# Performance work log

Measured on AMD Instinct MI355X. Metric: run time of the kernel, lower is better.

## Reference

```python
import jax, jax.numpy as jnp
import numpy as np

B, S, F = 128, 256, 40
H, D, NH, L, FF = 64, 128, 4, 2, 2048
REG, BIN, NW = 8, 1, 3
NEG = -1e9


def _ln(x, s, b, eps=1e-5):
    m = x.mean(-1, keepdims=True)
    v = ((x - m) ** 2).mean(-1, keepdims=True)
    return (x - m) / jnp.sqrt(v + eps) * s + b


def setup_inputs() -> dict:
    key = jax.random.key(0)
    ks = list(jax.random.split(key, 40))
    k = iter(ks)
    def rn(shape, s=0.05):
        return jax.random.normal(next(k), shape, jnp.float32) * s
    inp = {}
    inp['x'] = jax.random.normal(next(k), (B, S, F), jnp.float32)
    inp['mask'] = jnp.ones((B, S, F), jnp.float32)
    inp['delta'] = jax.random.uniform(next(k), (B, S, F), jnp.float32)
    # GRU params (torch layout: [3H, in], gates order r,z,n)
    inp['gru_w_ih'] = rn((3 * H, 3 * F))
    inp['gru_w_hh'] = rn((3 * H, H))
    inp['gru_b_ih'] = rn((3 * H,))
    inp['gru_b_hh'] = rn((3 * H,))
    inp['dm_w'] = rn((D, H)); inp['dm_b'] = rn((D,))
    # transformer layers stacked on leading dim L
    inp['in_proj_w'] = rn((L, 3 * D, D)); inp['in_proj_b'] = rn((L, 3 * D))
    inp['out_proj_w'] = rn((L, D, D)); inp['out_proj_b'] = rn((L, D))
    inp['lin1_w'] = rn((L, FF, D)); inp['lin1_b'] = rn((L, FF))
    inp['lin2_w'] = rn((L, D, FF)); inp['lin2_b'] = rn((L, D))
    inp['ln1_s'] = jnp.ones((L, D), jnp.float32); inp['ln1_b'] = jnp.zeros((L, D), jnp.float32)
    inp['ln2_s'] = jnp.ones((L, D), jnp.float32); inp['ln2_b'] = jnp.zeros((L, D), jnp.float32)
    inp['score_w'] = rn((1, D)); inp['score_b'] = rn((1,))
    inp['reg_w'] = rn((NW, REG, D)); inp['reg_b'] = rn((NW, REG))
    inp['bin_w'] = rn((NW, BIN, D)); inp['bin_b'] = rn((NW, BIN))
    inp['window_id'] = jax.random.randint(next(k), (B,), 0, NW, jnp.int32)
    return inp


def reference(x, mask, delta, gru_w_ih, gru_w_hh, gru_b_ih, gru_b_hh, dm_w, dm_b,
              in_proj_w, in_proj_b, out_proj_w, out_proj_b, lin1_w, lin1_b,
              lin2_w, lin2_b, ln1_s, ln1_b, ln2_s, ln2_b, score_w, score_b,
              reg_w, reg_b, bin_w, bin_b, window_id):
    inp = jnp.concatenate([x, mask, delta], -1)          # [B,S,3F]
    xw = inp @ gru_w_ih.T + gru_b_ih                      # [B,S,3H] precomputed input gates

    def step(h, xw_t):
        gh = h @ gru_w_hh.T + gru_b_hh
        xr, xz, xn = jnp.split(xw_t, 3, -1)
        hr, hz, hn = jnp.split(gh, 3, -1)
        r = jax.nn.sigmoid(xr + hr)
        zg = jax.nn.sigmoid(xz + hz)
        n = jnp.tanh(xn + r * hn)
        h_new = (1.0 - zg) * n + zg * h
        return h_new, h_new

    h0 = jnp.zeros((x.shape[0], H), x.dtype)
    _, hs = jax.lax.scan(step, h0, jnp.swapaxes(xw, 0, 1))  # [S,B,H]
    z = jnp.swapaxes(hs, 0, 1) @ dm_w.T + dm_b              # [B,S,D]

    time_mask = mask.sum(-1) > 0                            # [B,S] bool
    bias = jnp.where(time_mask[:, None, None, :], 0.0, NEG).astype(z.dtype)
    dh = D // NH
    scale = 1.0 / np.sqrt(dh)

    for l in range(L):  # post-LN torch TransformerEncoderLayer
        qkv = z @ in_proj_w[l].T + in_proj_b[l]
        q, k, v = jnp.split(qkv, 3, -1)
        q = q.reshape(B, S, NH, dh).transpose(0, 2, 1, 3)
        k = k.reshape(B, S, NH, dh).transpose(0, 2, 1, 3)
        v = v.reshape(B, S, NH, dh).transpose(0, 2, 1, 3)
        attn = jax.nn.softmax(jnp.einsum('bhqd,bhkd->bhqk', q, k) * scale + bias, -1)
        o = jnp.einsum('bhqk,bhkd->bhqd', attn, v).transpose(0, 2, 1, 3).reshape(B, S, D)
        z = _ln(z + (o @ out_proj_w[l].T + out_proj_b[l]), ln1_s[l], ln1_b[l])
        ff = jax.nn.relu(z @ lin1_w[l].T + lin1_b[l]) @ lin2_w[l].T + lin2_b[l]
        z = _ln(z + ff, ln2_s[l], ln2_b[l])

    scores = (z @ score_w.T + score_b)[..., 0]              # [B,S]
    scores = jnp.where(time_mask, scores, NEG)
    alpha = jax.nn.softmax(scores, 1)
    pooled = jnp.einsum('bsd,bs->bd', z, alpha)             # [B,D]

    # routed heads: gather 1-of-3 head weights per sample, batched matvec
    y_reg = jnp.einsum('bod,bd->bo', reg_w[window_id], pooled) + reg_b[window_id]
    y_bin = jnp.einsum('bod,bd->bo', bin_w[window_id], pooled) + bin_b[window_id]
    return (y_reg, y_bin)
```

## Files before the change

kernel.cpp:

```cpp
#include <hip/hip_runtime.h>

typedef __attribute__((ext_vector_type(8))) short short8;
typedef __attribute__((ext_vector_type(4))) float f32x4;
typedef unsigned short u16;

#define BB   128
#define SS   256
#define FIN  40
#define HH   64
#define DD   128
#define NHH  4
#define LL   2
#define NEGV (-1e9f)

__device__ __forceinline__ u16 f2b(float f) {
    unsigned u = __float_as_uint(f);
    return (u16)((u + 0x7FFFu + ((u >> 16) & 1u)) >> 16);
}
__device__ __forceinline__ float b2f(u16 u) {
    return __uint_as_float(((unsigned)u) << 16);
}

__global__ __launch_bounds__(256) void cvt_all_kernel(const float* __restrict__ dm_w,
                                                      const float* __restrict__ ip_w,
                                                      const float* __restrict__ op_w,
                                                      const float* __restrict__ l1_w,
                                                      const float* __restrict__ l2_w,
                                                      u16* __restrict__ o_dm, u16* __restrict__ o_ip,
                                                      u16* __restrict__ o_op, u16* __restrict__ o_l1,
                                                      u16* __restrict__ o_l2) {
    int blk = blockIdx.x;
    const float* s; u16* d; int off;
    if      (blk < 4)   { s = dm_w; d = o_dm; off = blk; }
    else if (blk < 52)  { s = ip_w; d = o_ip; off = blk - 4; }
    else if (blk < 68)  { s = op_w; d = o_op; off = blk - 52; }
    else if (blk < 324) { s = l1_w; d = o_l1; off = blk - 68; }
    else                { s = l2_w; d = o_l2; off = blk - 324; }
    int i = (off * 256 + threadIdx.x) * 8;
    float4 a = *(const float4*)&s[i];
    float4 b = *(const float4*)&s[i + 4];
    short8 o;
    o[0] = (short)f2b(a.x); o[1] = (short)f2b(a.y); o[2] = (short)f2b(a.z); o[3] = (short)f2b(a.w);
    o[4] = (short)f2b(b.x); o[5] = (short)f2b(b.y); o[6] = (short)f2b(b.z); o[7] = (short)f2b(b.w);
    *(short8*)&d[i] = o;
}

__global__ __launch_bounds__(256) void tm_kernel(const float* __restrict__ mask,
                                                 float* __restrict__ tm) {
    int i = blockIdx.x * blockDim.x + threadIdx.x;
    if (i >= BB * SS) return;
    const float* m = mask + (size_t)i * FIN;
    float s = 0.f;
    for (int f = 0; f < FIN; ++f) s += m[f];
    tm[i] = (s > 0.f) ? 1.f : 0.f;
}

__global__ __launch_bounds__(192) void xw_kernel(const float* __restrict__ x,
                                                 const float* __restrict__ mask,
                                                 const float* __restrict__ delta,
                                                 const float* __restrict__ w_ih,
                                                 const float* __restrict__ b_ih,
                                                 float* __restrict__ xwt) {
    __shared__ float inp[16][120];
    __shared__ float wl[192][21];
    int group = blockIdx.x >> 8;
    int t = blockIdx.x & 255;
    int tid = threadIdx.x;

    for (int idx = tid; idx < 16 * 120; idx += 192) {
        int r = idx / 120, k = idx % 120;
        size_t g = (size_t)(group * 16 + r) * 256 + t;
        float v;
        if (k < 40)      v = x[g * FIN + k];
        else if (k < 80) v = mask[g * FIN + (k - 40)];
        else             v = delta[g * FIN + (k - 80)];
        inp[r][k] = v;
    }

    float acc[16];
#pragma unroll
    for (int r = 0; r < 16; ++r) acc[r] = 0.f;

    for (int kt = 0; kt < 6; ++kt) {
        __syncthreads();
        for (int idx = tid; idx < 192 * 20; idx += 192) {
            int r = idx / 20, k = idx % 20;
            wl[r][k] = w_ih[(size_t)r * 120 + kt * 20 + k];
        }
        __syncthreads();
#pragma unroll
        for (int kk = 0; kk < 20; ++kk) {
            float w = wl[tid][kk];
            int kg = kt * 20 + kk;
#pragma unroll
            for (int r = 0; r < 16; ++r) acc[r] += w * inp[r][kg];
        }
    }
    float bias = b_ih[tid];
    float* o = xwt + ((size_t)(group * 256 + t) * 192 + tid) * 16;
#pragma unroll
    for (int r = 0; r < 16; r += 4) {
        float4 v = {acc[r] + bias, acc[r + 1] + bias, acc[r + 2] + bias, acc[r + 3] + bias};
        *(float4*)&o[r] = v;
    }
}

__device__ __forceinline__ float gru_gate(float xr, float xz, float xn,
                                          float ar, float az, float an, float hold) {
    float r  = 1.f / (1.f + __expf(-(xr + ar)));
    float zg = 1.f / (1.f + __expf(-(xz + az)));
    float nx = xn + r * an;
    float n  = 2.f / (1.f + __expf(-2.f * nx)) - 1.f;
    return (1.f - zg) * n + zg * hold;
}

__global__ __launch_bounds__(256, 1) void gru_scan_kernel(const float* __restrict__ w_hh,
                                                          const float* __restrict__ b_hh,
                                                          const float* __restrict__ xwt,
                                                          u16* __restrict__ hsb) {
    __shared__ __align__(16) u16 hb[2][16 * 64];
    int b0 = blockIdx.x * 16;
    int tid = threadIdx.x;
    int w = tid >> 6, lane = tid & 63;
    int fr = lane & 15, hi = lane >> 4;

    for (int idx = tid; idx < 1024; idx += 256) hb[0][idx] = 0;

    int c = w * 16 + fr;
    float br_ = b_hh[c], bz_ = b_hh[64 + c], bn_ = b_hh[128 + c];

    short8 wfr[2], wfz[2], wfn[2];
#pragma unroll
    for (int ks = 0; ks < 2; ++ks) {
        int slot = ks * 4 + hi;
        const float* p0 = w_hh + (size_t)c * 64 + slot * 8;
        const float* p1 = w_hh + (size_t)(64 + c) * 64 + slot * 8;
        const float* p2 = w_hh + (size_t)(128 + c) * 64 + slot * 8;
#pragma unroll
        for (int q = 0; q < 8; ++q) {
            wfr[ks][q] = (short)f2b(p0[q]);
            wfz[ks][q] = (short)f2b(p1[q]);
            wfn[ks][q] = (short)f2b(p2[q]);
        }
    }

    const float* xg = xwt + (size_t)blockIdx.x * (256 * 192 * 16);
    int lo = hi * 4;

    float hr0 = 0.f, hr1 = 0.f, hr2 = 0.f, hr3 = 0.f;

    int wo0 = (lo + 0) * 64 + ((((c >> 3) ^ ((lo + 0) & 7))) << 3) + (c & 7);
    int wo1 = (lo + 1) * 64 + ((((c >> 3) ^ ((lo + 1) & 7))) << 3) + (c & 7);
    int wo2 = (lo + 2) * 64 + ((((c >> 3) ^ ((lo + 2) & 7))) << 3) + (c & 7);
    int wo3 = (lo + 3) * 64 + ((((c >> 3) ^ ((lo + 3) & 7))) << 3) + (c & 7);
    size_t ho0 = ((size_t)(b0 + lo + 0) * SS) * 64 + c;
    size_t ho1 = ((size_t)(b0 + lo + 1) * SS) * 64 + c;
    size_t ho2 = ((size_t)(b0 + lo + 2) * SS) * 64 + c;
    size_t ho3 = ((size_t)(b0 + lo + 3) * SS) * 64 + c;

    float4 axr = *(const float4*)&xg[((size_t)0 * 192 + c) * 16 + lo];
    float4 axz = *(const float4*)&xg[((size_t)0 * 192 + 64 + c) * 16 + lo];
    float4 axn = *(const float4*)&xg[((size_t)0 * 192 + 128 + c) * 16 + lo];
    float4 bxr = *(const float4*)&xg[((size_t)1 * 192 + c) * 16 + lo];
    float4 bxz = *(const float4*)&xg[((size_t)1 * 192 + 64 + c) * 16 + lo];
    float4 bxn = *(const float4*)&xg[((size_t)1 * 192 + 128 + c) * 16 + lo];
    __syncthreads();

    int cur = 0;
    auto step = [&](float4 xr4, float4 xz4, float4 xn4, int t) {
        f32x4 ar = {br_, br_, br_, br_};
        f32x4 az = {bz_, bz_, bz_, bz_};
        f32x4 an = {bn_, bn_, bn_, bn_};
#pragma unroll
        for (int ks = 0; ks < 2; ++ks) {
            int soff = (((ks << 2) + hi) ^ (fr & 7)) << 3;
            short8 af = *(const short8*)&hb[cur][fr * 64 + soff];
            ar = __builtin_amdgcn_mfma_f32_16x16x32_bf16(af, wfr[ks], ar, 0, 0, 0);
            az = __builtin_amdgcn_mfma_f32_16x16x32_bf16(af, wfz[ks], az, 0, 0, 0);
            an = __builtin_amdgcn_mfma_f32_16x16x32_bf16(af, wfn[ks], an, 0, 0, 0);
        }
        hr0 = gru_gate(xr4.x, xz4.x, xn4.x, ar[0], az[0], an[0], hr0);
        hr1 = gru_gate(xr4.y, xz4.y, xn4.y, ar[1], az[1], an[1], hr1);
        hr2 = gru_gate(xr4.z, xz4.z, xn4.z, ar[2], az[2], an[2], hr2);
        hr3 = gru_gate(xr4.w, xz4.w, xn4.w, ar[3], az[3], an[3], hr3);
        u16 v0 = f2b(hr0), v1 = f2b(hr1), v2 = f2b(hr2), v3 = f2b(hr3);
        int nxt = cur ^ 1;
        hb[nxt][wo0] = v0; hb[nxt][wo1] = v1; hb[nxt][wo2] = v2; hb[nxt][wo3] = v3;
        hsb[ho0 + (size_t)t * 64] = v0;
        hsb[ho1 + (size_t)t * 64] = v1;
        hsb[ho2 + (size_t)t * 64] = v2;
        hsb[ho3 + (size_t)t * 64] = v3;
        asm volatile("s_waitcnt lgkmcnt(0)\n\ts_barrier" ::: "memory");
        cur = nxt;
    };

    for (int t = 0; t < SS; t += 2) {
        {
            int tp = (t + 2 < SS) ? t + 2 : t;
            float4 nr = *(const float4*)&xg[((size_t)tp * 192 + c) * 16 + lo];
            float4 nz = *(const float4*)&xg[((size_t)tp * 192 + 64 + c) * 16 + lo];
            float4 nn = *(const float4*)&xg[((size_t)tp * 192 + 128 + c) * 16 + lo];
            step(axr, axz, axn, t);
            axr = nr; axz = nz; axn = nn;
        }
        {
            int tp = (t + 3 < SS) ? t + 3 : t + 1;
            float4 nr = *(const float4*)&xg[((size_t)tp * 192 + c) * 16 + lo];
            float4 nz = *(const float4*)&xg[((size_t)tp * 192 + 64 + c) * 16 + lo];
            float4 nn = *(const float4*)&xg[((size_t)tp * 192 + 128 + c) * 16 + lo];
            step(bxr, bxz, bxn, t + 1);
            bxr = nr; bxz = nz; bxn = nn;
        }
    }
}

__device__ __forceinline__ void gl_lds16(const void* g, void* s) {
    __builtin_amdgcn_global_load_lds(
        (const __attribute__((address_space(1))) void*)g,
        (__attribute__((address_space(3))) void*)s, 16, 0, 0);
}

template <int MODE, bool RELU>
__global__ __launch_bounds__(256, 2) void mfma_gemm(const u16* __restrict__ A,
                                                    const u16* __restrict__ W,
                                                    const float* __restrict__ bias,
                                                    float* __restrict__ C,
                                                    u16* __restrict__ Cb,
                                                    const float* __restrict__ lns,
                                                    const float* __restrict__ lnb,
                                                    int M, int N, int K) {
    __shared__ __align__(16) u16 Al[128 * 64];
    __shared__ __align__(16) u16 Bl[128 * 64];
    __shared__ float lred[2][2][128];
    int bm = blockIdx.x, bn = blockIdx.y;
    int tid = threadIdx.x;
    int w = tid >> 6, lane = tid & 63;
    int wrow = (w >> 1) * 64, wcol = (w & 1) * 64;
    int fr = lane & 15, hi = lane >> 4;
    int rl = lane >> 3;
    int sl = lane & 7;
    int ssl = sl ^ rl;

    const u16* Ag = A + ((size_t)bm * 128) * K + ssl * 8;
    const u16* Wg = W + ((size_t)bn * 128) * K + ssl * 8;

    f32x4 acc[4][4];
#pragma unroll
    for (int i = 0; i < 4; ++i)
#pragma unroll
        for (int jj = 0; jj < 4; ++jj) acc[i][jj] = (f32x4){0.f, 0.f, 0.f, 0.f};

    int ar[4], br[4];
#pragma unroll
    for (int m = 0; m < 4; ++m) {
        ar[m] = (wrow + m * 16 + fr) * 64;
        br[m] = (wcol + m * 16 + fr) * 64;
    }
    int swz = (fr & 7);

    for (int kt = 0; kt < K; kt += 64) {
        __syncthreads();
#pragma unroll
        for (int i = 0; i < 4; ++i) {
            int c = w * 4 + i;
            int row = c * 8 + rl;
            gl_lds16(Ag + (size_t)row * K + kt, &Al[c * 512]);
            gl_lds16(Wg + (size_t)row * K + kt, &Bl[c * 512]);
        }
        __syncthreads();
#pragma unroll
        for (int kk = 0; kk < 2; ++kk) {
            short8 a[4], bq[4];
            int soff = (((kk << 2) + hi) ^ swz) << 3;
#pragma unroll
            for (int m = 0; m < 4; ++m)
                a[m] = *(const short8*)&Al[ar[m] + soff];
#pragma unroll
            for (int n = 0; n < 4; ++n)
                bq[n] = *(const short8*)&Bl[br[n] + soff];
#pragma unroll
            for (int m = 0; m < 4; ++m)
#pragma unroll
                for (int n = 0; n < 4; ++n)
                    acc[m][n] = __builtin_amdgcn_mfma_f32_16x16x32_bf16(a[m], bq[n], acc[m][n], 0, 0, 0);
        }
    }

    float bv[4];
#pragma unroll
    for (int n = 0; n < 4; ++n) bv[n] = bias[bn * 128 + wcol + n * 16 + fr];

    if (MODE == 4) {
        float v[4][4][4];
#pragma unroll
        for (int m = 0; m < 4; ++m)
#pragma unroll
            for (int j = 0; j < 4; ++j) {
                int row = bm * 128 + wrow + m * 16 + hi * 4 + j;
#pragma unroll
                for (int n = 0; n < 4; ++n)
                    v[m][n][j] = acc[m][n][j] + bv[n] + C[(size_t)row * 128 + wcol + n * 16 + fr];
            }
#pragma unroll
        for (int m = 0; m < 4; ++m)
#pragma unroll
            for (int j = 0; j < 4; ++j) {
                float s = v[m][0][j] + v[m][1][j] + v[m][2][j] + v[m][3][j];
                float q = v[m][0][j]*v[m][0][j] + v[m][1][j]*v[m][1][j]
                        + v[m][2][j]*v[m][2][j] + v[m][3][j]*v[m][3][j];
#pragma unroll
                for (int off = 1; off <= 8; off <<= 1) {
                    s += __shfl_xor(s, off);
                    q += __shfl_xor(q, off);
                }
                if (fr == 0) {
                    int lrow = wrow + m * 16 + hi * 4 + j;
                    lred[0][w & 1][lrow] = s;
                    lred[1][w & 1][lrow] = q;
                }
            }
        __syncthreads();
        float sv[4], bb[4];
#pragma unroll
        for (int n = 0; n < 4; ++n) {
            sv[n] = lns[wcol + n * 16 + fr];
            bb[n] = lnb[wcol + n * 16 + fr];
        }
#pragma unroll
        for (int m = 0; m < 4; ++m)
#pragma unroll
            for (int j = 0; j < 4; ++j) {
                int lrow = wrow + m * 16 + hi * 4 + j;
                float mean = (lred[0][0][lrow] + lred[0][1][lrow]) * (1.f / 128.f);
                float msq  = (lred[1][0][lrow] + lred[1][1][lrow]) * (1.f / 128.f);
                float rstd = rsqrtf(msq - mean * mean + 1e-5f);
                int row = bm * 128 + lrow;
#pragma unroll
                for (int n = 0; n < 4; ++n) {
                    int col = wcol + n * 16 + fr;
                    float o = (v[m][n][j] - mean) * rstd * sv[n] + bb[n];
                    C[(size_t)row * 128 + col] = o;
                    Cb[(size_t)row * 128 + col] = f2b(o);
                }
            }
    } else {
#pragma unroll
        for (int m = 0; m < 4; ++m) {
#pragma unroll
            for (int j = 0; j < 4; ++j) {
                int row = bm * 128 + wrow + m * 16 + hi * 4 + j;
#pragma unroll
                for (int n = 0; n < 4; ++n) {
                    int col = bn * 128 + wcol + n * 16 + fr;
                    float vv = acc[m][n][j] + bv[n];
                    if (RELU) vv = fmaxf(vv, 0.f);
                    if (MODE & 1) C[(size_t)row * N + col] = vv;
                    if (MODE & 2) Cb[(size_t)row * N + col] = f2b(vv);
                }
            }
        }
    }
}

__global__ __launch_bounds__(256, 1) void ff_fused_kernel(const u16* __restrict__ zbin,
                                                          const u16* __restrict__ w1,
                                                          const float* __restrict__ b1,
                                                          const u16* __restrict__ w2,
                                                          const float* __restrict__ b2,
                                                          const float* __restrict__ lns,
                                                          const float* __restrict__ lnb,
                                                          float* __restrict__ z,
                                                          u16* __restrict__ zbout) {
    __shared__ __align__(16) u16 ZB[2][128 * 64];
    __shared__ __align__(16) u16 W1C[2][128 * 64];
    __shared__ __align__(16) u16 W2C[2][128 * 64];
    __shared__ __align__(16) u16 A1[2][128 * 64];
    __shared__ float lred[2][2][128];
    int bm = blockIdx.x;
    int tid = threadIdx.x;
    int w = tid >> 6, lane = tid & 63;
    int wrow = (w >> 1) * 64, wcol = (w & 1) * 64;
    int fr = lane & 15, hi = lane >> 4;
    int rl = lane >> 3, ssl = (lane & 7) ^ rl;
    int swz = fr & 7;
    int xh = wrow >> 6;

#pragma unroll
    for (int hk = 0; hk < 2; ++hk)
#pragma unroll
        for (int i = 0; i < 4; ++i) {
            int ch = w * 4 + i, row = ch * 8 + rl;
            gl_lds16(zbin + ((size_t)(bm * 128 + row)) * 128 + hk * 64 + ssl * 8, &ZB[hk][ch * 512]);
        }

    f32x4 acc2[4][4];
#pragma unroll
    for (int m = 0; m < 4; ++m)
#pragma unroll
        for (int n = 0; n < 4; ++n) acc2[m][n] = (f32x4){0.f, 0.f, 0.f, 0.f};

    for (int ci = 0; ci < 16; ++ci) {
#pragma unroll
        for (int hk = 0; hk < 2; ++hk)
#pragma unroll
            for (int i = 0; i < 4; ++i) {
                int ch = w * 4 + i, row = ch * 8 + rl;
                gl_lds16(w1 + ((size_t)(ci * 128 + row)) * 128 + hk * 64 + ssl * 8, &W1C[hk][ch * 512]);
                gl_lds16(w2 + ((size_t)row) * 2048 + ci * 128 + hk * 64 + ssl * 8, &W2C[hk][ch * 512]);
            }
        __syncthreads();

        f32x4 acc1[4][4];
#pragma unroll
        for (int m = 0; m < 4; ++m)
#pragma unroll
            for (int n = 0; n < 4; ++n) acc1[m][n] = (f32x4){0.f, 0.f, 0.f, 0.f};
#pragma unroll
        for (int ks = 0; ks < 4; ++ks) {
            int hk = ks >> 1;
            int soff = ((((ks & 1) << 2) + hi) ^ swz) << 3;
            short8 a[4], b[4];
#pragma unroll
            for (int m = 0; m < 4; ++m)
                a[m] = *(const short8*)&W1C[hk][(wrow + m * 16 + fr) * 64 + soff];
#pragma unroll
            for (int n = 0; n < 4; ++n)
                b[n] = *(const short8*)&ZB[hk][(wcol + n * 16 + fr) * 64 + soff];
#pragma unroll
            for (int m = 0; m < 4; ++m)
#pragma unroll
                for (int n = 0; n < 4; ++n)
                    acc1[m][n] = __builtin_amdgcn_mfma_f32_16x16x32_bf16(a[m], b[n], acc1[m][n], 0, 0, 0);
        }
#pragma unroll
        for (int m = 0; m < 4; ++m) {
            int x0 = wrow + m * 16 + hi * 4;
            float4 bb = *(const float4*)&b1[ci * 128 + x0];
            int slot = (x0 & 63) >> 3;
            int wadd = x0 & 7;
#pragma unroll
            for (int n = 0; n < 4; ++n) {
                int r = wcol + n * 16 + fr;
                float v0 = fmaxf(acc1[m][n][0] + bb.x, 0.f);
                float v1 = fmaxf(acc1[m][n][1] + bb.y, 0.f);
                float v2 = fmaxf(acc1[m][n][2] + bb.z, 0.f);
                float v3 = fmaxf(acc1[m][n][3] + bb.w, 0.f);
                uint2 pk;
                pk.x = (unsigned)f2b(v0) | ((unsigned)f2b(v1) << 16);
                pk.y = (unsigned)f2b(v2) | ((unsigned)f2b(v3) << 16);
                *(uint2*)&A1[xh][r * 64 + ((slot ^ (r & 7)) << 3) + wadd] = pk;
            }
        }
        __syncthreads();

#pragma unroll
        for (int ks = 0; ks < 4; ++ks) {
            int hk = ks >> 1;
            int soff = ((((ks & 1) << 2) + hi) ^ swz) << 3;
            short8 a[4], b[4];
#pragma unroll
            for (int m = 0; m < 4; ++m)
                a[m] = *(const short8*)&W2C[hk][(wrow + m * 16 + fr) * 64 + soff];
#pragma unroll
            for (int n = 0; n < 4; ++n)
                b[n] = *(const short8*)&A1[hk][(wcol + n * 16 + fr) * 64 + soff];
#pragma unroll
            for (int m = 0; m < 4; ++m)
#pragma unroll
                for (int n = 0; n < 4; ++n)
                    acc2[m][n] = __builtin_amdgcn_mfma_f32_16x16x32_bf16(a[m], b[n], acc2[m][n], 0, 0, 0);
        }
        __syncthreads();
    }

    float vv[4][4][4];
#pragma unroll
    for (int m = 0; m < 4; ++m) {
        int x0 = wrow + m * 16 + hi * 4;
        float4 bb = *(const float4*)&b2[x0];
#pragma unroll
        for (int n = 0; n < 4; ++n) {
            int y = wcol + n * 16 + fr;
            float4 zo = *(const float4*)&z[((size_t)(bm * 128 + y)) * 128 + x0];
            vv[m][n][0] = acc2[m][n][0] + bb.x + zo.x;
            vv[m][n][1] = acc2[m][n][1] + bb.y + zo.y;
            vv[m][n][2] = acc2[m][n][2] + bb.z + zo.z;
            vv[m][n][3] = acc2[m][n][3] + bb.w + zo.w;
        }
    }
#pragma unroll
    for (int n = 0; n < 4; ++n) {
        float s = 0.f, q = 0.f;
#pragma unroll
        for (int m = 0; m < 4; ++m)
#pragma unroll
            for (int j = 0; j < 4; ++j) { float v = vv[m][n][j]; s += v; q += v * v; }
        s += __shfl_xor(s, 16); s += __shfl_xor(s, 32);
        q += __shfl_xor(q, 16); q += __shfl_xor(q, 32);
        if (hi == 0) {
            int y = wcol + n * 16 + fr;
            lred[0][xh][y] = s;
            lred[1][xh][y] = q;
        }
    }
    __syncthreads();
#pragma unroll
    for (int n = 0; n < 4; ++n) {
        int y = wcol + n * 16 + fr;
        float mean = (lred[0][0][y] + lred[0][1][y]) * (1.f / 128.f);
        float msq  = (lred[1][0][y] + lred[1][1][y]) * (1.f / 128.f);
        float rstd = rsqrtf(msq - mean * mean + 1e-5f);
#pragma unroll
        for (int m = 0; m < 4; ++m) {
            int x0 = wrow + m * 16 + hi * 4;
            float4 sv = *(const float4*)&lns[x0];
            float4 bv = *(const float4*)&lnb[x0];
            float o0 = (vv[m][n][0] - mean) * rstd * sv.x + bv.x;
            float o1 = (vv[m][n][1] - mean) * rstd * sv.y + bv.y;
            float o2 = (vv[m][n][2] - mean) * rstd * sv.z + bv.z;
            float o3 = (vv[m][n][3] - mean) * rstd * sv.w + bv.w;
            size_t zoff = ((size_t)(bm * 128 + y)) * 128 + x0;
            *(float4*)&z[zoff] = (float4){o0, o1, o2, o3};
            uint2 pk;
            pk.x = (unsigned)f2b(o0) | ((unsigned)f2b(o1) << 16);
            pk.y = (unsigned)f2b(o2) | ((unsigned)f2b(o3) << 16);
            *(uint2*)&zbout[zoff] = pk;
        }
    }
}

__global__ __launch_bounds__(256) void attn_mfma_kernel(const u16* __restrict__ qkv,
                                                        const float* __restrict__ tm,
                                                        u16* __restrict__ attno) {
    __shared__ __align__(16) u16 Kl[256 * 40];
    __shared__ __align__(16) u16 Vt[32 * 264];
    __shared__ __align__(16) u16 Pl[4][64 * 72];
    __shared__ float tmb[256];
    int bh = blockIdx.x;
    int b = bh >> 2, hd = bh & 3;
    int tid = threadIdx.x;
    int w = tid >> 6, lane = tid & 63;
    int fr = lane & 15, hi = lane >> 4;
    const u16* base = qkv + (size_t)b * SS * 384 + hd * 32;

    for (int idx = tid; idx < 1024; idx += 256) {
        int r = idx >> 2, s = idx & 3;
        short8 v = *(const short8*)(base + (size_t)r * 384 + 128 + s * 8);
        *(short8*)&Kl[r * 40 + s * 8] = v;
    }
    for (int idx = tid; idx < 1024; idx += 256) {
        int r = idx >> 2, s = idx & 3;
        short8 v = *(const short8*)(base + (size_t)r * 384 + 256 + s * 8);
#pragma unroll
        for (int q = 0; q < 8; ++q) Vt[(s * 8 + q) * 264 + r] = (u16)v[q];
    }
    tmb[tid] = (tm[b * SS + tid] > 0.f) ? 0.f : NEGV;

    int q0 = w * 64;
    short8 qf[4];
#pragma unroll
    for (int m = 0; m < 4; ++m)
        qf[m] = *(const short8*)(base + (size_t)(q0 + m * 16 + fr) * 384 + hi * 8);
    __syncthreads();

    const float scale = 0.17677669529663687f;
    f32x4 accO[4][2];
#pragma unroll
    for (int m = 0; m < 4; ++m) {
        accO[m][0] = (f32x4){0.f, 0.f, 0.f, 0.f};
        accO[m][1] = (f32x4){0.f, 0.f, 0.f, 0.f};
    }
    float den[4][4];
#pragma unroll
    for (int m = 0; m < 4; ++m)
#pragma unroll
        for (int j = 0; j < 4; ++j) den[m][j] = 0.f;

    u16* pw = &Pl[w][0];

    for (int kt = 0; kt < 4; ++kt) {
        f32x4 accS[4][4];
#pragma unroll
        for (int m = 0; m < 4; ++m)
#pragma unroll
            for (int n = 0; n < 4; ++n) accS[m][n] = (f32x4){0.f, 0.f, 0.f, 0.f};
        short8 kf[4];
#pragma unroll
        for (int n = 0; n < 4; ++n)
            kf[n] = *(const short8*)&Kl[(kt * 64 + n * 16 + fr) * 40 + hi * 8];
#pragma unroll
        for (int m = 0; m < 4; ++m)
#pragma unroll
            for (int n = 0; n < 4; ++n)
                accS[m][n] = __builtin_amdgcn_mfma_f32_16x16x32_bf16(qf[m], kf[n], accS[m][n], 0, 0, 0);

        float bias[4];
#pragma unroll
        for (int n = 0; n < 4; ++n) bias[n] = tmb[kt * 64 + n * 16 + fr];

#pragma unroll
        for (int m = 0; m < 4; ++m) {
            float rs0 = 0.f, rs1 = 0.f, rs2 = 0.f, rs3 = 0.f;
#pragma unroll
            for (int n = 0; n < 4; ++n) {
                float p0 = __expf(accS[m][n][0] * scale + bias[n]);
                float p1 = __expf(accS[m][n][1] * scale + bias[n]);
                float p2 = __expf(accS[m][n][2] * scale + bias[n]);
                float p3 = __expf(accS[m][n][3] * scale + bias[n]);
                rs0 += p0; rs1 += p1; rs2 += p2; rs3 += p3;
                int cb = n * 16 + fr;
                pw[(m * 16 + hi * 4 + 0) * 72 + cb] = f2b(p0);
                pw[(m * 16 + hi * 4 + 1) * 72 + cb] = f2b(p1);
                pw[(m * 16 + hi * 4 + 2) * 72 + cb] = f2b(p2);
                pw[(m * 16 + hi * 4 + 3) * 72 + cb] = f2b(p3);
            }
#pragma unroll
            for (int off = 1; off <= 8; off <<= 1) {
                rs0 += __shfl_xor(rs0, off);
                rs1 += __shfl_xor(rs1, off);
                rs2 += __shfl_xor(rs2, off);
                rs3 += __shfl_xor(rs3, off);
            }
            den[m][0] += rs0; den[m][1] += rs1; den[m][2] += rs2; den[m][3] += rs3;
        }
        asm volatile("s_waitcnt lgkmcnt(0)" ::: "memory");

#pragma unroll
        for (int ks = 0; ks < 2; ++ks) {
            short8 pf[4], vf[2];
#pragma unroll
            for (int m = 0; m < 4; ++m)
                pf[m] = *(const short8*)&pw[(m * 16 + fr) * 72 + ks * 32 + hi * 8];
#pragma unroll
            for (int nd = 0; nd < 2; ++nd)
                vf[nd] = *(const short8*)&Vt[(nd * 16 + fr) * 264 + kt * 64 + ks * 32 + hi * 8];
#pragma unroll
            for (int m = 0; m < 4; ++m)
#pragma unroll
                for (int nd = 0; nd < 2; ++nd)
                    accO[m][nd] = __builtin_amdgcn_mfma_f32_16x16x32_bf16(pf[m], vf[nd], accO[m][nd], 0, 0, 0);
        }
    }

    u16* orow = attno + (size_t)(b * SS + q0) * DD + hd * 32;
#pragma unroll
    for (int m = 0; m < 4; ++m)
#pragma unroll
        for (int j = 0; j < 4; ++j) {
            float inv = 1.f / den[m][j];
            int qr = m * 16 + hi * 4 + j;
            orow[(size_t)qr * DD + fr]      = f2b(accO[m][0][j] * inv);
            orow[(size_t)qr * DD + 16 + fr] = f2b(accO[m][1][j] * inv);
        }
}

__global__ __launch_bounds__(256) void score_kernel(const float* __restrict__ z,
                                                    const float* __restrict__ score_w,
                                                    const float* __restrict__ score_b,
                                                    const float* __restrict__ tm,
                                                    float* __restrict__ scores) {
    int row = blockIdx.x * 64 + (threadIdx.x >> 2);
    int c = threadIdx.x & 3;
    const float* zr = z + (size_t)row * DD + c * 32;
    const float* wr = score_w + c * 32;
    float acc = 0.f;
#pragma unroll
    for (int j = 0; j < 32; j += 4) {
        float4 a = *(const float4*)(zr + j), w = *(const float4*)(wr + j);
        acc += a.x * w.x + a.y * w.y + a.z * w.z + a.w * w.w;
    }
    acc += __shfl_xor(acc, 1);
    acc += __shfl_xor(acc, 2);
    if (c == 0) {
        float sc = acc + score_b[0];
        scores[row] = (tm[row] > 0.f) ? sc : NEGV;
    }
}

__global__ __launch_bounds__(256) void pool_kernel(const float* __restrict__ z,
                                                   const float* __restrict__ scores,
                                                   float* __restrict__ pooled) {
    int b = blockIdx.x;
    int tid = threadIdx.x;
    __shared__ float al[SS];
    __shared__ float red[8];
    __shared__ float pp[2][128];

    float sc = scores[b * SS + tid];
    float m = sc;
#pragma unroll
    for (int off = 32; off; off >>= 1) m = fmaxf(m, __shfl_xor(m, off));
    if ((tid & 63) == 0) red[tid >> 6] = m;
    __syncthreads();
    m = fmaxf(fmaxf(red[0], red[1]), fmaxf(red[2], red[3]));
    float e = __expf(sc - m);
    float ssum = e;
#pragma unroll
    for (int off = 32; off; off >>= 1) ssum += __shfl_xor(ssum, off);
    if ((tid & 63) == 0) red[4 + (tid >> 6)] = ssum;
    __syncthreads();
    ssum = red[4] + red[5] + red[6] + red[7];
    al[tid] = e / ssum;
    __syncthreads();

    int d = tid & 127, half = tid >> 7;
    float acc = 0.f;
    for (int t = half; t < SS; t += 2) acc += al[t] * z[((size_t)b * SS + t) * DD + d];
    pp[half][d] = acc;
    __syncthreads();
    if (tid < 128) pooled[b * 128 + tid] = pp[0][tid] + pp[1][tid];
}

__global__ __launch_bounds__(128) void head_kernel(const float* __restrict__ pooled,
                                                   const float* __restrict__ reg_w,
                                                   const float* __restrict__ reg_b,
                                                   const float* __restrict__ bin_w,
                                                   const float* __restrict__ bin_b,
                                                   const int* __restrict__ wid,
                                                   float* __restrict__ out) {
    int b = blockIdx.x, tid = threadIdx.x;
    __shared__ float p[128];
    p[tid] = pooled[b * 128 + tid];
    __syncthreads();
    if (tid < 9) {
        int w = wid[b];
        const float* wrow;
        float bias;
        if (tid < 8) { wrow = reg_w + ((size_t)w * 8 + tid) * 128; bias = reg_b[w * 8 + tid]; }
        else         { wrow = bin_w + (size_t)w * 128;             bias = bin_b[w]; }
        float acc = bias;
        for (int k = 0; k < 128; ++k) acc += wrow[k] * p[k];
        if (tid < 8) out[b * 8 + tid] = acc;
        else         out[1024 + b] = acc;
    }
}

extern "C" void kernel_launch(void* const* d_in, const int* in_sizes, int n_in,
                              void* d_out, int out_size, void* d_ws, size_t ws_size,
                              hipStream_t stream) {
    const float* x         = (const float*)d_in[0];
    const float* mask      = (const float*)d_in[1];
    const float* delta     = (const float*)d_in[2];
    const float* gru_w_ih  = (const float*)d_in[3];
    const float* gru_w_hh  = (const float*)d_in[4];
    const float* gru_b_ih  = (const float*)d_in[5];
    const float* gru_b_hh  = (const float*)d_in[6];
    const float* dm_w      = (const float*)d_in[7];
    const float* dm_b      = (const float*)d_in[8];
    const float* in_proj_w = (const float*)d_in[9];
    const float* in_proj_b = (const float*)d_in[10];
    const float* out_proj_w= (const float*)d_in[11];
    const float* out_proj_b= (const float*)d_in[12];
    const float* lin1_w    = (const float*)d_in[13];
    const float* lin1_b    = (const float*)d_in[14];
    const float* lin2_w    = (const float*)d_in[15];
    const float* lin2_b    = (const float*)d_in[16];
    const float* ln1_s     = (const float*)d_in[17];
    const float* ln1_bb    = (const float*)d_in[18];
    const float* ln2_s     = (const float*)d_in[19];
    const float* ln2_bb    = (const float*)d_in[20];
    const float* score_w   = (const float*)d_in[21];
    const float* score_b   = (const float*)d_in[22];
    const float* reg_w     = (const float*)d_in[23];
    const float* reg_b     = (const float*)d_in[24];
    const float* bin_w     = (const float*)d_in[25];
    const float* bin_b     = (const float*)d_in[26];
    const int*   window_id = (const int*)d_in[27];
    float* out = (float*)d_out;

    char* w8 = (char*)d_ws;
    float* z      = (float*)(w8 + 0);
    u16*   zb     = (u16*)  (w8 + 16777216);
    u16*   hsb    = (u16*)  (w8 + 25165824);
    u16*   wb_dm  = (u16*)  (w8 + 29360128);
    u16*   wb_ip  = (u16*)  (w8 + 29376512);
    u16*   wb_op  = (u16*)  (w8 + 29573120);
    u16*   wb_l1  = (u16*)  (w8 + 29638656);
    u16*   wb_l2  = (u16*)  (w8 + 30687232);
    float* tm     = (float*)(w8 + 31735808);
    float* scores = (float*)(w8 + 31866880);
    float* pooled = (float*)(w8 + 31997952);
    float* xwt    = (float*)(w8 + 32063488);
    u16*   qkvb   = (u16*)  (w8 + 32063488);
    u16*   attnob = (u16*)  (w8 + 57229312);

    cvt_all_kernel<<<580, 256, 0, stream>>>(dm_w, in_proj_w, out_proj_w, lin1_w, lin2_w,
                                            wb_dm, wb_ip, wb_op, wb_l1, wb_l2);

    tm_kernel<<<(BB * SS + 255) / 256, 256, 0, stream>>>(mask, tm);
    xw_kernel<<<2048, 192, 0, stream>>>(x, mask, delta, gru_w_ih, gru_b_ih, xwt);
    gru_scan_kernel<<<8, 256, 0, stream>>>(gru_w_hh, gru_b_hh, xwt, hsb);

    mfma_gemm<3, false><<<dim3(256, 1), 256, 0, stream>>>(
        hsb, wb_dm, dm_b, z, zb, nullptr, nullptr, 32768, 128, 64);

    for (int l = 0; l < LL; ++l) {
        mfma_gemm<2, false><<<dim3(256, 3), 256, 0, stream>>>(
            zb, wb_ip + (size_t)l * 49152, in_proj_b + l * 384, nullptr, qkvb,
            nullptr, nullptr, 32768, 384, 128);
        attn_mfma_kernel<<<BB * NHH, 256, 0, stream>>>(qkvb, tm, attnob);
        mfma_gemm<4, false><<<dim3(256, 1), 256, 0, stream>>>(
            attnob, wb_op + (size_t)l * 16384, out_proj_b + l * 128, z, zb,
            ln1_s + l * 128, ln1_bb + l * 128, 32768, 128, 128);
        ff_fused_kernel<<<256, 256, 0, stream>>>(
            zb, wb_l1 + (size_t)l * 262144, lin1_b + l * 2048,
            wb_l2 + (size_t)l * 262144, lin2_b + l * 128,
            ln2_s + l * 128, ln2_bb + l * 128, z, zb);
    }

    score_kernel<<<BB * SS / 64, 256, 0, stream>>>(z, score_w, score_b, tm, scores);
    pool_kernel<<<BB, 256, 0, stream>>>(z, scores, pooled);
    head_kernel<<<BB, 128, 0, stream>>>(pooled, reg_w, reg_b, bin_w, bin_b, window_id, out);
}
```

Baseline: 561.7 us.

## Split GRU gate work across 8 waves and fuse score, pool and head kernels

The GRU scan block grows from 4 to 8 wavefronts. Each pair of waves repeats the same MFMA recurrence, but each wave evaluates the gate nonlinearities for only 2 of the 4 batch rows, which shortens the serial per-step elementwise critical path. The score, softmax-pool and routed-head kernels are merged into one per-batch kernel, removing two launches and the round trips of scores and pooled vectors through global memory. The trade-offs are duplicated MFMA work, a barrier spanning more waves on every step, and a serial 128-length dot product per thread in the fused score stage.

```diff
diff --git a/kernel.cpp b/kernel.cpp
--- a/kernel.cpp
+++ b/kernel.cpp
@@ -114,7 +114,7 @@
     return (1.f - zg) * n + zg * hold;
 }
 
-__global__ __launch_bounds__(256, 1) void gru_scan_kernel(const float* __restrict__ w_hh,
+__global__ __launch_bounds__(512, 1) void gru_scan_kernel(const float* __restrict__ w_hh,
                                                           const float* __restrict__ b_hh,
                                                           const float* __restrict__ xwt,
                                                           u16* __restrict__ hsb) {
@@ -123,10 +123,12 @@
     int tid = threadIdx.x;
     int w = tid >> 6, lane = tid & 63;
     int fr = lane & 15, hi = lane >> 4;
-
-    for (int idx = tid; idx < 1024; idx += 256) hb[0][idx] = 0;
-
-    int c = w * 16 + fr;
+    int cw = w & 3;
+    int jg = w >> 2;
+
+    for (int idx = tid; idx < 1024; idx += 512) hb[0][idx] = 0;
+
+    int c = cw * 16 + fr;
     float br_ = b_hh[c], bz_ = b_hh[64 + c], bn_ = b_hh[128 + c];
 
     short8 wfr[2], wfz[2], wfn[2];
@@ -145,29 +147,25 @@
     }
 
     const float* xg = xwt + (size_t)blockIdx.x * (256 * 192 * 16);
-    int lo = hi * 4;
-
-    float hr0 = 0.f, hr1 = 0.f, hr2 = 0.f, hr3 = 0.f;
-
-    int wo0 = (lo + 0) * 64 + ((((c >> 3) ^ ((lo + 0) & 7))) << 3) + (c & 7);
-    int wo1 = (lo + 1) * 64 + ((((c >> 3) ^ ((lo + 1) & 7))) << 3) + (c & 7);
-    int wo2 = (lo + 2) * 64 + ((((c >> 3) ^ ((lo + 2) & 7))) << 3) + (c & 7);
-    int wo3 = (lo + 3) * 64 + ((((c >> 3) ^ ((lo + 3) & 7))) << 3) + (c & 7);
-    size_t ho0 = ((size_t)(b0 + lo + 0) * SS) * 64 + c;
-    size_t ho1 = ((size_t)(b0 + lo + 1) * SS) * 64 + c;
-    size_t ho2 = ((size_t)(b0 + lo + 2) * SS) * 64 + c;
-    size_t ho3 = ((size_t)(b0 + lo + 3) * SS) * 64 + c;
-
-    float4 axr = *(const float4*)&xg[((size_t)0 * 192 + c) * 16 + lo];
-    float4 axz = *(const float4*)&xg[((size_t)0 * 192 + 64 + c) * 16 + lo];
-    float4 axn = *(const float4*)&xg[((size_t)0 * 192 + 128 + c) * 16 + lo];
-    float4 bxr = *(const float4*)&xg[((size_t)1 * 192 + c) * 16 + lo];
-    float4 bxz = *(const float4*)&xg[((size_t)1 * 192 + 64 + c) * 16 + lo];
-    float4 bxn = *(const float4*)&xg[((size_t)1 * 192 + 128 + c) * 16 + lo];
+    int lo = hi * 4 + jg * 2;
+
+    float hrA = 0.f, hrB = 0.f;
+
+    int woA = (lo + 0) * 64 + ((((c >> 3) ^ ((lo + 0) & 7))) << 3) + (c & 7);
+    int woB = (lo + 1) * 64 + ((((c >> 3) ^ ((lo + 1) & 7))) << 3) + (c & 7);
+    size_t hoA = ((size_t)(b0 + lo + 0) * SS) * 64 + c;
+    size_t hoB = ((size_t)(b0 + lo + 1) * SS) * 64 + c;
+
+    float2 axr = *(const float2*)&xg[((size_t)0 * 192 + c) * 16 + lo];
+    float2 axz = *(const float2*)&xg[((size_t)0 * 192 + 64 + c) * 16 + lo];
+    float2 axn = *(const float2*)&xg[((size_t)0 * 192 + 128 + c) * 16 + lo];
+    float2 bxr = *(const float2*)&xg[((size_t)1 * 192 + c) * 16 + lo];
+    float2 bxz = *(const float2*)&xg[((size_t)1 * 192 + 64 + c) * 16 + lo];
+    float2 bxn = *(const float2*)&xg[((size_t)1 * 192 + 128 + c) * 16 + lo];
     __syncthreads();
 
     int cur = 0;
-    auto step = [&](float4 xr4, float4 xz4, float4 xn4, int t) {
+    auto step = [&](float2 xr2, float2 xz2, float2 xn2, int t) {
         f32x4 ar = {br_, br_, br_, br_};
         f32x4 az = {bz_, bz_, bz_, bz_};
         f32x4 an = {bn_, bn_, bn_, bn_};
@@ -179,17 +177,16 @@
             az = __builtin_amdgcn_mfma_f32_16x16x32_bf16(af, wfz[ks], az, 0, 0, 0);
             an = __builtin_amdgcn_mfma_f32_16x16x32_bf16(af, wfn[ks], an, 0, 0, 0);
         }
-        hr0 = gru_gate(xr4.x, xz4.x, xn4.x, ar[0], az[0], an[0], hr0);
-        hr1 = gru_gate(xr4.y, xz4.y, xn4.y, ar[1], az[1], an[1], hr1);
-        hr2 = gru_gate(xr4.z, xz4.z, xn4.z, ar[2], az[2], an[2], hr2);
-        hr3 = gru_gate(xr4.w, xz4.w, xn4.w, ar[3], az[3], an[3], hr3);
-        u16 v0 = f2b(hr0), v1 = f2b(hr1), v2 = f2b(hr2), v3 = f2b(hr3);
+        float aR0, aR1, aZ0, aZ1, aN0, aN1;
+        if (jg == 0) { aR0 = ar[0]; aR1 = ar[1]; aZ0 = az[0]; aZ1 = az[1]; aN0 = an[0]; aN1 = an[1]; }
+        else         { aR0 = ar[2]; aR1 = ar[3]; aZ0 = az[2]; aZ1 = az[3]; aN0 = an[2]; aN1 = an[3]; }
+        hrA = gru_gate(xr2.x, xz2.x, xn2.x, aR0, aZ0, aN0, hrA);
+        hrB = gru_gate(xr2.y, xz2.y, xn2.y, aR1, aZ1, aN1, hrB);
+        u16 v0 = f2b(hrA), v1 = f2b(hrB);
         int nxt = cur ^ 1;
-        hb[nxt][wo0] = v0; hb[nxt][wo1] = v1; hb[nxt][wo2] = v2; hb[nxt][wo3] = v3;
-        hsb[ho0 + (size_t)t * 64] = v0;
-        hsb[ho1 + (size_t)t * 64] = v1;
-        hsb[ho2 + (size_t)t * 64] = v2;
-        hsb[ho3 + (size_t)t * 64] = v3;
+        hb[nxt][woA] = v0; hb[nxt][woB] = v1;
+        hsb[hoA + (size_t)t * 64] = v0;
+        hsb[hoB + (size_t)t * 64] = v1;
         asm volatile("s_waitcnt lgkmcnt(0)\n\ts_barrier" ::: "memory");
         cur = nxt;
     };
@@ -197,17 +194,17 @@
     for (int t = 0; t < SS; t += 2) {
         {
             int tp = (t + 2 < SS) ? t + 2 : t;
-            float4 nr = *(const float4*)&xg[((size_t)tp * 192 + c) * 16 + lo];
-            float4 nz = *(const float4*)&xg[((size_t)tp * 192 + 64 + c) * 16 + lo];
-            float4 nn = *(const float4*)&xg[((size_t)tp * 192 + 128 + c) * 16 + lo];
+            float2 nr = *(const float2*)&xg[((size_t)tp * 192 + c) * 16 + lo];
+            float2 nz = *(const float2*)&xg[((size_t)tp * 192 + 64 + c) * 16 + lo];
+            float2 nn = *(const float2*)&xg[((size_t)tp * 192 + 128 + c) * 16 + lo];
             step(axr, axz, axn, t);
             axr = nr; axz = nz; axn = nn;
         }
         {
             int tp = (t + 3 < SS) ? t + 3 : t + 1;
-            float4 nr = *(const float4*)&xg[((size_t)tp * 192 + c) * 16 + lo];
-            float4 nz = *(const float4*)&xg[((size_t)tp * 192 + 64 + c) * 16 + lo];
-            float4 nn = *(const float4*)&xg[((size_t)tp * 192 + 128 + c) * 16 + lo];
+            float2 nr = *(const float2*)&xg[((size_t)tp * 192 + c) * 16 + lo];
+            float2 nz = *(const float2*)&xg[((size_t)tp * 192 + 64 + c) * 16 + lo];
+            float2 nn = *(const float2*)&xg[((size_t)tp * 192 + 128 + c) * 16 + lo];
             step(bxr, bxz, bxn, t + 1);
             bxr = nr; bxz = nz; bxn = nn;
         }
@@ -654,39 +651,38 @@
         }
 }
 
-__global__ __launch_bounds__(256) void score_kernel(const float* __restrict__ z,
-                                                    const float* __restrict__ score_w,
-                                                    const float* __restrict__ score_b,
-                                                    const float* __restrict__ tm,
-                                                    float* __restrict__ scores) {
-    int row = blockIdx.x * 64 + (threadIdx.x >> 2);
-    int c = threadIdx.x & 3;
-    const float* zr = z + (size_t)row * DD + c * 32;
-    const float* wr = score_w + c * 32;
-    float acc = 0.f;
-#pragma unroll
-    for (int j = 0; j < 32; j += 4) {
-        float4 a = *(const float4*)(zr + j), w = *(const float4*)(wr + j);
-        acc += a.x * w.x + a.y * w.y + a.z * w.z + a.w * w.w;
-    }
-    acc += __shfl_xor(acc, 1);
-    acc += __shfl_xor(acc, 2);
-    if (c == 0) {
-        float sc = acc + score_b[0];
-        scores[row] = (tm[row] > 0.f) ? sc : NEGV;
-    }
-}
-
-__global__ __launch_bounds__(256) void pool_kernel(const float* __restrict__ z,
-                                                   const float* __restrict__ scores,
-                                                   float* __restrict__ pooled) {
+__global__ __launch_bounds__(256) void pool_all_kernel(const float* __restrict__ z,
+                                                       const float* __restrict__ score_w,
+                                                       const float* __restrict__ score_b,
+                                                       const float* __restrict__ tm,
+                                                       const float* __restrict__ reg_w,
+                                                       const float* __restrict__ reg_b,
+                                                       const float* __restrict__ bin_w,
+                                                       const float* __restrict__ bin_b,
+                                                       const int* __restrict__ wid,
+                                                       float* __restrict__ out) {
     int b = blockIdx.x;
     int tid = threadIdx.x;
+    __shared__ float sw[128];
     __shared__ float al[SS];
     __shared__ float red[8];
     __shared__ float pp[2][128];
-
-    float sc = scores[b * SS + tid];
+    __shared__ float p[128];
+
+    if (tid < 128) sw[tid] = score_w[tid];
+    __syncthreads();
+
+    const float* zr = z + ((size_t)b * SS + tid) * DD;
+    float acc = 0.f;
+#pragma unroll
+    for (int j = 0; j < 128; j += 4) {
+        float4 a = *(const float4*)&zr[j];
+        float4 wv = *(const float4*)&sw[j];
+        acc += a.x * wv.x + a.y * wv.y + a.z * wv.z + a.w * wv.w;
+    }
+    float sc = acc + score_b[0];
+    sc = (tm[b * SS + tid] > 0.f) ? sc : NEGV;
+
     float m = sc;
 #pragma unroll
     for (int off = 32; off; off >>= 1) m = fmaxf(m, __shfl_xor(m, off));
@@ -704,34 +700,23 @@
     __syncthreads();
 
     int d = tid & 127, half = tid >> 7;
-    float acc = 0.f;
-    for (int t = half; t < SS; t += 2) acc += al[t] * z[((size_t)b * SS + t) * DD + d];
-    pp[half][d] = acc;
-    __syncthreads();
-    if (tid < 128) pooled[b * 128 + tid] = pp[0][tid] + pp[1][tid];
-}
-
-__global__ __launch_bounds__(128) void head_kernel(const float* __restrict__ pooled,
-                                                   const float* __restrict__ reg_w,
-                                                   const float* __restrict__ reg_b,
-                                                   const float* __restrict__ bin_w,
-                                                   const float* __restrict__ bin_b,
-                                                   const int* __restrict__ wid,
-                                                   float* __restrict__ out) {
-    int b = blockIdx.x, tid = threadIdx.x;
-    __shared__ float p[128];
-    p[tid] = pooled[b * 128 + tid];
-    __syncthreads();
+    float pa = 0.f;
+    for (int t = half; t < SS; t += 2) pa += al[t] * z[((size_t)b * SS + t) * DD + d];
+    pp[half][d] = pa;
+    __syncthreads();
+    if (tid < 128) p[tid] = pp[0][tid] + pp[1][tid];
+    __syncthreads();
+
     if (tid < 9) {
-        int w = wid[b];
+        int wi = wid[b];
         const float* wrow;
         float bias;
-        if (tid < 8) { wrow = reg_w + ((size_t)w * 8 + tid) * 128; bias = reg_b[w * 8 + tid]; }
-        else         { wrow = bin_w + (size_t)w * 128;             bias = bin_b[w]; }
-        float acc = bias;
-        for (int k = 0; k < 128; ++k) acc += wrow[k] * p[k];
-        if (tid < 8) out[b * 8 + tid] = acc;
-        else         out[1024 + b] = acc;
+        if (tid < 8) { wrow = reg_w + ((size_t)wi * 8 + tid) * 128; bias = reg_b[wi * 8 + tid]; }
+        else         { wrow = bin_w + (size_t)wi * 128;             bias = bin_b[wi]; }
+        float hacc = bias;
+        for (int k = 0; k < 128; ++k) hacc += wrow[k] * p[k];
+        if (tid < 8) out[b * 8 + tid] = hacc;
+        else         out[1024 + b] = hacc;
     }
 }
 
@@ -778,8 +763,6 @@
     u16*   wb_l1  = (u16*)  (w8 + 29638656);
     u16*   wb_l2  = (u16*)  (w8 + 30687232);
     float* tm     = (float*)(w8 + 31735808);
-    float* scores = (float*)(w8 + 31866880);
-    float* pooled = (float*)(w8 + 31997952);
     float* xwt    = (float*)(w8 + 32063488);
     u16*   qkvb   = (u16*)  (w8 + 32063488);
     u16*   attnob = (u16*)  (w8 + 57229312);
@@ -789,7 +772,7 @@
 
     tm_kernel<<<(BB * SS + 255) / 256, 256, 0, stream>>>(mask, tm);
     xw_kernel<<<2048, 192, 0, stream>>>(x, mask, delta, gru_w_ih, gru_b_ih, xwt);
-    gru_scan_kernel<<<8, 256, 0, stream>>>(gru_w_hh, gru_b_hh, xwt, hsb);
+    gru_scan_kernel<<<8, 512, 0, stream>>>(gru_w_hh, gru_b_hh, xwt, hsb);
 
     mfma_gemm<3, false><<<dim3(256, 1), 256, 0, stream>>>(
         hsb, wb_dm, dm_b, z, zb, nullptr, nullptr, 32768, 128, 64);
@@ -808,7 +791,6 @@
             ln2_s + l * 128, ln2_bb + l * 128, z, zb);
     }
 
-    score_kernel<<<BB * SS / 64, 256, 0, stream>>>(z, score_w, score_b, tm, scores);
-    pool_kernel<<<BB, 256, 0, stream>>>(z, scores, pooled);
-    head_kernel<<<BB, 128, 0, stream>>>(pooled, reg_w, reg_b, bin_w, bin_b, window_id, out);
-}
+    pool_all_kernel<<<BB, 256, 0, stream>>>(z, score_w, score_b, tm,
+                                            reg_w, reg_b, bin_w, bin_b, window_id, out);
+}
```

Result: faster. 544.4 us (-3.1%).
